# Optimization experiments

Measured on AMD Instinct MI355X. Metric: run time of the kernel, lower is better.

## Reference

```python
import jax, jax.numpy as jnp
import numpy as np

B, M, IN_DIM, D, H, NL = 4, 2048, 512, 1024, 4, 2
HD = D // H           # head_dim = 256
HD2 = HD // 2
ROPE_BASE = 10000.0
LN_EPS = 1e-5


def setup_inputs() -> dict:
    key = jax.random.key(0)
    ks = jax.random.split(key, 9)
    s = 0.02
    return {
        "x": jax.random.normal(ks[0], (B, M, IN_DIM), jnp.float32),
        "positions": jnp.sort(jax.random.randint(ks[1], (B, M), 0, 8192), axis=-1).astype(jnp.int32),
        "mask": jnp.ones((B, M), jnp.float32),
        "in_w": jax.random.normal(ks[2], (IN_DIM, D), jnp.float32) * s,
        "in_b": jnp.zeros((D,), jnp.float32),
        "qkv_w": jax.random.normal(ks[3], (NL, D, 3 * D), jnp.float32) * s,
        "o_w": jax.random.normal(ks[4], (NL, D, D), jnp.float32) * s,
        "ln1_g": jnp.ones((NL, D), jnp.float32),
        "ln1_b": jnp.zeros((NL, D), jnp.float32),
        "ffn_w1": jax.random.normal(ks[5], (NL, D, 4 * D), jnp.float32) * s,
        "ffn_b1": jnp.zeros((NL, 4 * D), jnp.float32),
        "ffn_w2": jax.random.normal(ks[6], (NL, 4 * D, D), jnp.float32) * s,
        "ffn_b2": jnp.zeros((NL, D), jnp.float32),
        "ln2_g": jnp.ones((NL, D), jnp.float32),
        "ln2_b": jnp.zeros((NL, D), jnp.float32),
        "start_state": jax.random.normal(ks[7], (D,), jnp.float32) * 0.02,
    }


def _layernorm(x, g, b):
    mu = jnp.mean(x, axis=-1, keepdims=True)
    var = jnp.mean((x - mu) ** 2, axis=-1, keepdims=True)
    return (x - mu) * jax.lax.rsqrt(var + LN_EPS) * g + b


def _rope_cos_sin(positions):
    # rope_module(pos): angles over head_dim//2 freqs, shared across heads
    inv_freq = 1.0 / (ROPE_BASE ** (jnp.arange(HD2, dtype=jnp.float32) * 2.0 / HD))
    ang = positions.astype(jnp.float32)[:, :, None] * inv_freq  # (B, L, HD2)
    return jnp.cos(ang), jnp.sin(ang)


def _apply_rotary(x, cos, sin):
    # x: (B, H, L, HD); cos/sin: (B, 1, L, HD2) broadcast over heads
    x1, x2 = x[..., :HD2], x[..., HD2:]
    return jnp.concatenate([x1 * cos - x2 * sin, x1 * sin + x2 * cos], axis=-1)


def _self_attention(x, cos, sin, mask, qkv_w, o_w):
    Bx, L, Dx = x.shape
    qkv = (x @ qkv_w).reshape(Bx, L, 3, H, HD)
    q = jnp.transpose(qkv[:, :, 0], (0, 2, 1, 3))  # (B, H, L, HD)
    k = jnp.transpose(qkv[:, :, 1], (0, 2, 1, 3))
    v = jnp.transpose(qkv[:, :, 2], (0, 2, 1, 3))
    q = _apply_rotary(q, cos, sin)
    k = _apply_rotary(k, cos, sin)
    scores = jnp.einsum("bhqd,bhkd->bhqk", q, k) * (1.0 / np.sqrt(HD))
    scores = jnp.where(mask[:, None, None, :] == 0, -jnp.inf, scores)
    attn = jax.nn.softmax(scores, axis=-1)
    out = jnp.einsum("bhqk,bhkd->bhqd", attn, v)
    out = jnp.transpose(out, (0, 2, 1, 3)).reshape(Bx, L, Dx)
    return out @ o_w


def reference(x, positions, mask, in_w, in_b, qkv_w, o_w, ln1_g, ln1_b,
              ffn_w1, ffn_b1, ffn_w2, ffn_b2, ln2_g, ln2_b, start_state):
    h = x @ in_w + in_b  # (B, M, D)
    cos, sin = _rope_cos_sin(positions)
    cos, sin = cos[:, None], sin[:, None]  # (B, 1, M, HD2)
    for l in range(NL):
        h = h + _self_attention(_layernorm(h, ln1_g[l], ln1_b[l]), cos, sin, mask,
                                qkv_w[l], o_w[l])
        y = _layernorm(h, ln2_g[l], ln2_b[l])
        y = jax.nn.gelu(y @ ffn_w1[l] + ffn_b1[l], approximate=False) @ ffn_w2[l] + ffn_b2[l]
        h = h + y
    lengths = jnp.sum(mask, axis=1)
    last_idx = jnp.clip(lengths.astype(jnp.int32) - 1, 0, None)
    gathered = h[jnp.arange(h.shape[0]), last_idx]  # (B, D)
    has_hist = lengths > 0
    return jnp.where(has_hist[:, None], gathered, start_state[None, :])
```

## Files before the change

### kernel.cpp

```cpp
#include <hip/hip_runtime.h>
#include <math.h>

typedef __attribute__((ext_vector_type(8))) short bf16x8;
typedef __attribute__((ext_vector_type(4))) float floatx4;
typedef __attribute__((ext_vector_type(4))) unsigned short ushort4v;

typedef __attribute__((address_space(1))) void as1_void;
typedef __attribute__((address_space(3))) void as3_void;

static __device__ __forceinline__ unsigned short f2b(float f) {
    union { float f; unsigned u; } v; v.f = f;
    unsigned r = v.u + 0x7fffu + ((v.u >> 16) & 1u);
    return (unsigned short)(r >> 16);
}
static __device__ __forceinline__ float b2f(unsigned short h) {
    union { unsigned u; float f; } v; v.u = ((unsigned)h) << 16;
    return v.f;
}

template<int TM, int TN>
__global__ __launch_bounds__(256) void gemm_bf16(
    const unsigned short* __restrict__ A,
    const unsigned short* __restrict__ Bt,
    float* __restrict__ Cf, unsigned short* __restrict__ Cb,
    const float* __restrict__ bias,
    int K, int lda, int ldb, int ldc,
    int zdiv, long a_s1, long a_s2, long b_s1, long b_s2, long c_s1, long c_s2,
    int mode)
{
    constexpr int FM  = TM / 32;
    constexpr int FN  = TN / 32;
    constexpr int NRA = TM / 64;
    constexpr int NRB = TN / 64;
    constexpr int NSTG = NRA + NRB;

    __shared__ unsigned short As[2][4 * TM * 8];
    __shared__ unsigned short Bs[2][4 * TN * 8];

    const int tid  = threadIdx.x;
    const int wid  = tid >> 6;
    const int lane = tid & 63;
    const int q    = lane >> 4;
    const int r    = lane & 15;

    const int z  = blockIdx.z;
    const int zq = z / zdiv, zr = z % zdiv;
    const long offC = (long)zq * c_s1 + (long)zr * c_s2;

    const int m0 = blockIdx.y * TM;
    const int n0 = blockIdx.x * TN;

    const unsigned short* Ab = A  + (long)zq * a_s1 + (long)zr * a_s2 + (long)m0 * lda;
    const unsigned short* Bb = Bt + (long)zq * b_s1 + (long)zr * b_s2 + (long)n0 * ldb;

    const int wr = (wid >> 1) * (TM / 2);
    const int wc = (wid & 1)  * (TN / 2);

    floatx4 acc[FM][FN];
    #pragma unroll
    for (int i = 0; i < FM; ++i)
        #pragma unroll
        for (int j = 0; j < FN; ++j)
            acc[i][j] = (floatx4){0.f, 0.f, 0.f, 0.f};

    const int qc = wid;
    const int nk = K >> 5;

    auto stage = [&](int kt, int buf) {
        const int kofs = (kt << 5) + (qc << 3);
        #pragma unroll
        for (int rb = 0; rb < NRA; ++rb)
            __builtin_amdgcn_global_load_lds(
                (as1_void*)(void*)(Ab + (long)(lane + rb * 64) * lda + kofs),
                (as3_void*)&As[buf][(qc * TM + rb * 64) * 8], 16, 0, 0);
        #pragma unroll
        for (int rb = 0; rb < NRB; ++rb)
            __builtin_amdgcn_global_load_lds(
                (as1_void*)(void*)(Bb + (long)(lane + rb * 64) * ldb + kofs),
                (as3_void*)&Bs[buf][(qc * TN + rb * 64) * 8], 16, 0, 0);
    };

    stage(0, 0);
    for (int kt = 0; kt < nk; ++kt) {
        const int cur = kt & 1;
        if (kt + 1 < nk) {
            stage(kt + 1, cur ^ 1);
            if constexpr (NSTG == 2)      asm volatile("s_waitcnt vmcnt(2)" ::: "memory");
            else if constexpr (NSTG == 4) asm volatile("s_waitcnt vmcnt(4)" ::: "memory");
            else if constexpr (NSTG == 6) asm volatile("s_waitcnt vmcnt(6)" ::: "memory");
            else                          asm volatile("s_waitcnt vmcnt(0)" ::: "memory");
        } else {
            asm volatile("s_waitcnt vmcnt(0)" ::: "memory");
        }
        asm volatile("s_barrier" ::: "memory");

        bf16x8 av[FM], bv[FN];
        #pragma unroll
        for (int i = 0; i < FM; ++i)
            av[i] = *(const bf16x8*)&As[cur][(q * TM + wr + i * 16 + r) * 8];
        #pragma unroll
        for (int j = 0; j < FN; ++j)
            bv[j] = *(const bf16x8*)&Bs[cur][(q * TN + wc + j * 16 + r) * 8];
        #pragma unroll
        for (int i = 0; i < FM; ++i)
            #pragma unroll
            for (int j = 0; j < FN; ++j)
                acc[i][j] = __builtin_amdgcn_mfma_f32_16x16x32_bf16(av[i], bv[j], acc[i][j], 0, 0, 0);

        asm volatile("s_waitcnt lgkmcnt(0)" ::: "memory");
        asm volatile("s_barrier" ::: "memory");
    }

    #pragma unroll
    for (int i = 0; i < FM; ++i) {
        const int gr0 = m0 + wr + i * 16 + q * 4;
        #pragma unroll
        for (int j = 0; j < FN; ++j) {
            const int gc = n0 + wc + j * 16 + r;
            const float bvl = bias ? bias[gc] : 0.0f;
            #pragma unroll
            for (int rr = 0; rr < 4; ++rr) {
                const long cidx = offC + (long)(gr0 + rr) * ldc + gc;
                float v = acc[i][j][rr] + bvl;
                if (mode == 0) {
                    Cf[cidx] = v;
                } else if (mode == 1) {
                    Cf[cidx] += v;
                } else if (mode == 2) {
                    Cb[cidx] = f2b(v);
                } else {
                    Cb[cidx] = f2b(0.5f * v * (1.0f + erff(v * 0.70710678118654752f)));
                }
            }
        }
    }
}

__global__ void transpose_cast_f32(const float* __restrict__ in, unsigned short* __restrict__ out,
                                   int R, int C)
{
    __shared__ float t[32][33];
    const int c0 = blockIdx.x * 32, r0 = blockIdx.y * 32;
    const int tx = threadIdx.x, ty = threadIdx.y;
    #pragma unroll
    for (int i = 0; i < 4; ++i)
        t[ty + i * 8][tx] = in[(long)(r0 + ty + i * 8) * C + c0 + tx];
    __syncthreads();
    #pragma unroll
    for (int i = 0; i < 4; ++i)
        out[(long)(c0 + ty + i * 8) * R + r0 + tx] = f2b(t[tx][ty + i * 8]);
}

__global__ void transpose_v(const unsigned short* __restrict__ qkv, unsigned short* __restrict__ vT)
{
    __shared__ unsigned short t[32][33];
    const int hh = blockIdx.z;
    const int d0 = blockIdx.x * 32, m0 = blockIdx.y * 32;
    const int tx = threadIdx.x, ty = threadIdx.y;
    const unsigned short* ip = qkv + 2048 + hh * 256;
    unsigned short* op = vT + (long)hh * 524288;
    #pragma unroll
    for (int i = 0; i < 4; ++i)
        t[ty + i * 8][tx] = ip[(long)(m0 + ty + i * 8) * 3072 + d0 + tx];
    __syncthreads();
    #pragma unroll
    for (int i = 0; i < 4; ++i)
        op[(long)(d0 + ty + i * 8) * 2048 + m0 + tx] = t[tx][ty + i * 8];
}

__global__ void cast_f32_bf16(const float* __restrict__ in, unsigned short* __restrict__ out)
{
    const long i = (long)blockIdx.x * 256 + threadIdx.x;
    const float4 v = ((const float4*)in)[i];
    ushort4v o;
    o[0] = f2b(v.x); o[1] = f2b(v.y); o[2] = f2b(v.z); o[3] = f2b(v.w);
    ((ushort4v*)out)[i] = o;
}

__global__ void zero_f32(float* __restrict__ p)
{
    p[blockIdx.x * 256 + threadIdx.x] = 0.0f;
}

__global__ __launch_bounds__(256) void ln_kernel(const float* __restrict__ h,
    const float* __restrict__ g, const float* __restrict__ bta,
    unsigned short* __restrict__ out)
{
    const int tok = blockIdx.x;
    const float4 v = ((const float4*)(h + (long)tok * 1024))[threadIdx.x];
    float s  = v.x + v.y + v.z + v.w;
    float s2 = v.x * v.x + v.y * v.y + v.z * v.z + v.w * v.w;
    #pragma unroll
    for (int off = 32; off > 0; off >>= 1) {
        s  += __shfl_xor(s, off);
        s2 += __shfl_xor(s2, off);
    }
    __shared__ float rs[4], rs2[4];
    const int wid = threadIdx.x >> 6, lane = threadIdx.x & 63;
    if (lane == 0) { rs[wid] = s; rs2[wid] = s2; }
    __syncthreads();
    s  = rs[0] + rs[1] + rs[2] + rs[3];
    s2 = rs2[0] + rs2[1] + rs2[2] + rs2[3];
    const float mu = s * (1.0f / 1024.0f);
    float var = s2 * (1.0f / 1024.0f) - mu * mu;
    var = fmaxf(var, 0.0f);
    const float rsg = 1.0f / sqrtf(var + 1e-5f);
    const float4 gv = ((const float4*)g)[threadIdx.x];
    const float4 bv = ((const float4*)bta)[threadIdx.x];
    ushort4v o;
    o[0] = f2b((v.x - mu) * rsg * gv.x + bv.x);
    o[1] = f2b((v.y - mu) * rsg * gv.y + bv.y);
    o[2] = f2b((v.z - mu) * rsg * gv.z + bv.z);
    o[3] = f2b((v.w - mu) * rsg * gv.w + bv.w);
    *(ushort4v*)&out[(long)tok * 1024 + threadIdx.x * 4] = o;
}

__global__ __launch_bounds__(256) void rope_kernel(unsigned short* __restrict__ qkv,
                                                   const int* __restrict__ pos)
{
    const int tok = blockIdx.x;
    const float p = (float)pos[tok];
    unsigned short* base = qkv + (long)tok * 3072;
    const float kC = -13.287712379549449f / 128.0f;
    #pragma unroll
    for (int it = 0; it < 2; ++it) {
        const int idx = threadIdx.x + it * 256;
        const int hh = idx >> 7, d = idx & 127;
        const float inv = exp2f((float)d * kC);
        const float ang = p * inv;
        const float c = cosf(ang), s = sinf(ang);
        unsigned short* qp = base + hh * 256 + d;
        {
            const float x1 = b2f(qp[0]), x2 = b2f(qp[128]);
            qp[0]   = f2b(x1 * c - x2 * s);
            qp[128] = f2b(x1 * s + x2 * c);
        }
        unsigned short* kp = qp + 1024;
        {
            const float x1 = b2f(kp[0]), x2 = b2f(kp[128]);
            kp[0]   = f2b(x1 * c - x2 * s);
            kp[128] = f2b(x1 * s + x2 * c);
        }
    }
}

__global__ __launch_bounds__(256) void softmax_kernel(unsigned short* __restrict__ sc,
                                                      const float* __restrict__ mrow)
{
    unsigned short* row = sc + (long)blockIdx.x * 2048;
    const int t = threadIdx.x;

    float v[8];
    const ushort4v u0 = *(const ushort4v*)&row[t * 8];
    const ushort4v u1 = *(const ushort4v*)&row[t * 8 + 4];
    #pragma unroll
    for (int i = 0; i < 4; ++i) { v[i] = b2f(u0[i]); v[4 + i] = b2f(u1[i]); }

    const float4 m0 = ((const float4*)mrow)[t * 2];
    const float4 m1 = ((const float4*)mrow)[t * 2 + 1];
    float mk[8] = {m0.x, m0.y, m0.z, m0.w, m1.x, m1.y, m1.z, m1.w};

    float mx = -3.0e38f;
    #pragma unroll
    for (int i = 0; i < 8; ++i) {
        v[i] = (mk[i] == 0.0f) ? -3.0e38f : v[i] * 0.0625f;
        mx = fmaxf(mx, v[i]);
    }
    #pragma unroll
    for (int off = 32; off > 0; off >>= 1) mx = fmaxf(mx, __shfl_xor(mx, off));
    __shared__ float rmx[4], rsm[4];
    const int wid = t >> 6, lane = t & 63;
    if (lane == 0) rmx[wid] = mx;
    __syncthreads();
    mx = fmaxf(fmaxf(rmx[0], rmx[1]), fmaxf(rmx[2], rmx[3]));

    float s = 0.0f;
    #pragma unroll
    for (int i = 0; i < 8; ++i) { v[i] = expf(v[i] - mx); s += v[i]; }
    #pragma unroll
    for (int off = 32; off > 0; off >>= 1) s += __shfl_xor(s, off);
    if (lane == 0) rsm[wid] = s;
    __syncthreads();
    s = rsm[0] + rsm[1] + rsm[2] + rsm[3];
    const float invs = (s > 0.0f) ? 1.0f / s : 0.0f;

    ushort4v o0, o1;
    #pragma unroll
    for (int i = 0; i < 4; ++i) { o0[i] = f2b(v[i] * invs); o1[i] = f2b(v[4 + i] * invs); }
    *(ushort4v*)&row[t * 8]     = o0;
    *(ushort4v*)&row[t * 8 + 4] = o1;
}

__global__ __launch_bounds__(256) void gather_kernel(const float* __restrict__ h,
    const float* __restrict__ mask, const float* __restrict__ ss, float* __restrict__ out)
{
    const int b = blockIdx.x;
    const float* mrow = mask + b * 2048;
    const int t = threadIdx.x;
    float s = 0.0f;
    #pragma unroll
    for (int i = 0; i < 8; ++i) s += mrow[t * 8 + i];
    #pragma unroll
    for (int off = 32; off > 0; off >>= 1) s += __shfl_xor(s, off);
    __shared__ float red[4];
    if ((t & 63) == 0) red[t >> 6] = s;
    __syncthreads();
    const float len = red[0] + red[1] + red[2] + red[3];
    const int L = (int)len;
    const int last = (L > 0) ? (L - 1) : 0;
    const bool has = len > 0.0f;
    const float* src = has ? (h + ((long)b * 2048 + last) * 1024) : ss;
    #pragma unroll
    for (int i = 0; i < 4; ++i) {
        const int d = t + i * 256;
        out[b * 1024 + d] = src[d];
    }
}

extern "C" void kernel_launch(void* const* d_in, const int* in_sizes, int n_in,
                              void* d_out, int out_size, void* d_ws, size_t ws_size,
                              hipStream_t stream)
{
    (void)in_sizes; (void)n_in; (void)out_size;
    const float* x      = (const float*)d_in[0];
    const int*   pos    = (const int*)d_in[1];
    const float* mask   = (const float*)d_in[2];
    const float* in_w   = (const float*)d_in[3];
    const float* in_b   = (const float*)d_in[4];
    const float* qkv_w  = (const float*)d_in[5];
    const float* o_w    = (const float*)d_in[6];
    const float* ln1_g  = (const float*)d_in[7];
    const float* ln1_b  = (const float*)d_in[8];
    const float* ffn_w1 = (const float*)d_in[9];
    const float* ffn_b1 = (const float*)d_in[10];
    const float* ffn_w2 = (const float*)d_in[11];
    const float* ffn_b2 = (const float*)d_in[12];
    const float* ln2_g  = (const float*)d_in[13];
    const float* ln2_b  = (const float*)d_in[14];
    const float* sstate = (const float*)d_in[15];
    float* out = (float*)d_out;

    const size_t NEED = 143654912ull;
    if (ws_size < NEED) {
        zero_f32<<<16, 256, 0, stream>>>(out);
        return;
    }
    char* w = (char*)d_ws;
    unsigned short* wt_in  = (unsigned short*)(w);
    unsigned short* wt_qkv = (unsigned short*)(w + 1048576);
    unsigned short* wt_o   = (unsigned short*)(w + 7340032);
    unsigned short* wt_f1  = (unsigned short*)(w + 9437184);
    unsigned short* wt_f2  = (unsigned short*)(w + 17825792);
    float*          hbuf   = (float*)(w + 26214400);
    unsigned short* xn_bf  = (unsigned short*)(w + 59768832);
    unsigned short* ao_bf  = (unsigned short*)(w + 76546048);
    unsigned short* qkv_b  = (unsigned short*)(w + 93323264);
    unsigned short* vT_b   = (unsigned short*)(w + 105906176);
    unsigned short* scmid  = (unsigned short*)(w + 110100480);
    unsigned short* x_bf   = ao_bf;
    unsigned short* mid_bf = (unsigned short*)(w + 76546048);

    const dim3 tb(32, 8);

    transpose_cast_f32<<<dim3(32, 16), tb, 0, stream>>>(in_w, wt_in, 512, 1024);
    cast_f32_bf16<<<4096, 256, 0, stream>>>(x, x_bf);

    gemm_bf16<128,128><<<dim3(8, 64, 1), 256, 0, stream>>>(x_bf, wt_in, hbuf, nullptr, in_b,
        512, 512, 512, 1024, 1, 0, 0, 0, 0, 0, 0, 0);

    for (int l = 0; l < 2; ++l) {
        transpose_cast_f32<<<dim3(96, 32),  tb, 0, stream>>>(qkv_w  + (long)l * 3145728, wt_qkv, 1024, 3072);
        transpose_cast_f32<<<dim3(32, 32),  tb, 0, stream>>>(o_w    + (long)l * 1048576, wt_o,   1024, 1024);
        transpose_cast_f32<<<dim3(128, 32), tb, 0, stream>>>(ffn_w1 + (long)l * 4194304, wt_f1,  1024, 4096);
        transpose_cast_f32<<<dim3(32, 128), tb, 0, stream>>>(ffn_w2 + (long)l * 4194304, wt_f2,  4096, 1024);

        ln_kernel<<<8192, 256, 0, stream>>>(hbuf, ln1_g + l * 1024, ln1_b + l * 1024, xn_bf);

        for (int b = 0; b < 4; ++b) {
            gemm_bf16<64,64><<<dim3(48, 32, 1), 256, 0, stream>>>(xn_bf + (long)b * 2097152, wt_qkv,
                nullptr, qkv_b, nullptr, 1024, 1024, 1024, 3072, 1, 0, 0, 0, 0, 0, 0, 2);
            rope_kernel<<<2048, 256, 0, stream>>>(qkv_b, pos + b * 2048);
            transpose_v<<<dim3(8, 64, 4), tb, 0, stream>>>(qkv_b, vT_b);
            gemm_bf16<128,128><<<dim3(16, 16, 4), 256, 0, stream>>>(qkv_b, qkv_b + 1024,
                nullptr, scmid, nullptr, 256, 3072, 3072, 2048,
                1, 256l, 0, 256l, 0, 4194304l, 0, 2);
            softmax_kernel<<<8192, 256, 0, stream>>>(scmid, mask + b * 2048);
            gemm_bf16<64,64><<<dim3(4, 32, 4), 256, 0, stream>>>(scmid, vT_b,
                nullptr, ao_bf + (long)b * 2097152, nullptr, 2048, 2048, 2048, 1024,
                1, 4194304l, 0, 524288l, 0, 256l, 0, 2);
        }
        gemm_bf16<128,128><<<dim3(8, 64, 1), 256, 0, stream>>>(ao_bf, wt_o,
            hbuf, nullptr, nullptr, 1024, 1024, 1024, 1024, 1, 0, 0, 0, 0, 0, 0, 1);

        ln_kernel<<<8192, 256, 0, stream>>>(hbuf, ln2_g + l * 1024, ln2_b + l * 1024, xn_bf);

        gemm_bf16<256,128><<<dim3(32, 32, 1), 256, 0, stream>>>(xn_bf, wt_f1,
            nullptr, mid_bf, ffn_b1 + l * 4096, 1024, 1024, 1024, 4096, 1, 0, 0, 0, 0, 0, 0, 3);
        gemm_bf16<128,128><<<dim3(8, 64, 1), 256, 0, stream>>>(mid_bf, wt_f2,
            hbuf, nullptr, ffn_b2 + l * 1024, 4096, 4096, 4096, 1024, 1, 0, 0, 0, 0, 0, 0, 1);
    }

    gather_kernel<<<4, 256, 0, stream>>>(hbuf, mask, sstate, out);
}
```

Before: 2.516 ms.

## Retune GEMM tile shapes and make layernorm one token per wavefront

Several GEMM launches switch to different tile shapes: in-proj, o-proj and FFN2 go to 128x64, QKV goes to 64x128, and FFN1 goes to 128x128. The main intent is more workgroups per launch and better CU occupancy. The layernorm kernel now handles one token per 64-lane wavefront with four tokens per block, which removes the LDS reduction and __syncthreads. The vmcnt wait table gains an NSTG==3 case (needed for the new tile combos) and drops NSTG==6. Smaller tiles trade load balance for less data reuse per tile.

```diff
diff --git a/kernel.cpp b/kernel.cpp
--- a/kernel.cpp
+++ b/kernel.cpp
@@ -86,8 +86,8 @@
         if (kt + 1 < nk) {
             stage(kt + 1, cur ^ 1);
             if constexpr (NSTG == 2)      asm volatile("s_waitcnt vmcnt(2)" ::: "memory");
+            else if constexpr (NSTG == 3) asm volatile("s_waitcnt vmcnt(3)" ::: "memory");
             else if constexpr (NSTG == 4) asm volatile("s_waitcnt vmcnt(4)" ::: "memory");
-            else if constexpr (NSTG == 6) asm volatile("s_waitcnt vmcnt(6)" ::: "memory");
             else                          asm volatile("s_waitcnt vmcnt(0)" ::: "memory");
         } else {
             asm volatile("s_waitcnt vmcnt(0)" ::: "memory");
@@ -186,33 +186,40 @@
     const float* __restrict__ g, const float* __restrict__ bta,
     unsigned short* __restrict__ out)
 {
-    const int tok = blockIdx.x;
-    const float4 v = ((const float4*)(h + (long)tok * 1024))[threadIdx.x];
-    float s  = v.x + v.y + v.z + v.w;
-    float s2 = v.x * v.x + v.y * v.y + v.z * v.z + v.w * v.w;
+    const int wid  = threadIdx.x >> 6;
+    const int lane = threadIdx.x & 63;
+    const long tok = (long)blockIdx.x * 4 + wid;
+    const float4* h4 = (const float4*)(h + tok * 1024);
+
+    float4 v[4];
+    float s = 0.f, s2 = 0.f;
+    #pragma unroll
+    for (int i = 0; i < 4; ++i) {
+        v[i] = h4[lane + i * 64];
+        s  += v[i].x + v[i].y + v[i].z + v[i].w;
+        s2 += v[i].x * v[i].x + v[i].y * v[i].y + v[i].z * v[i].z + v[i].w * v[i].w;
+    }
     #pragma unroll
     for (int off = 32; off > 0; off >>= 1) {
         s  += __shfl_xor(s, off);
         s2 += __shfl_xor(s2, off);
     }
-    __shared__ float rs[4], rs2[4];
-    const int wid = threadIdx.x >> 6, lane = threadIdx.x & 63;
-    if (lane == 0) { rs[wid] = s; rs2[wid] = s2; }
-    __syncthreads();
-    s  = rs[0] + rs[1] + rs[2] + rs[3];
-    s2 = rs2[0] + rs2[1] + rs2[2] + rs2[3];
     const float mu = s * (1.0f / 1024.0f);
     float var = s2 * (1.0f / 1024.0f) - mu * mu;
     var = fmaxf(var, 0.0f);
     const float rsg = 1.0f / sqrtf(var + 1e-5f);
-    const float4 gv = ((const float4*)g)[threadIdx.x];
-    const float4 bv = ((const float4*)bta)[threadIdx.x];
-    ushort4v o;
-    o[0] = f2b((v.x - mu) * rsg * gv.x + bv.x);
-    o[1] = f2b((v.y - mu) * rsg * gv.y + bv.y);
-    o[2] = f2b((v.z - mu) * rsg * gv.z + bv.z);
-    o[3] = f2b((v.w - mu) * rsg * gv.w + bv.w);
-    *(ushort4v*)&out[(long)tok * 1024 + threadIdx.x * 4] = o;
+
+    #pragma unroll
+    for (int i = 0; i < 4; ++i) {
+        const float4 gv = ((const float4*)g)[lane + i * 64];
+        const float4 bv = ((const float4*)bta)[lane + i * 64];
+        ushort4v o;
+        o[0] = f2b((v[i].x - mu) * rsg * gv.x + bv.x);
+        o[1] = f2b((v[i].y - mu) * rsg * gv.y + bv.y);
+        o[2] = f2b((v[i].z - mu) * rsg * gv.z + bv.z);
+        o[3] = f2b((v[i].w - mu) * rsg * gv.w + bv.w);
+        *(ushort4v*)&out[tok * 1024 + (lane + i * 64) * 4] = o;
+    }
 }
 
 __global__ __launch_bounds__(256) void rope_kernel(unsigned short* __restrict__ qkv,
@@ -365,7 +372,7 @@
     transpose_cast_f32<<<dim3(32, 16), tb, 0, stream>>>(in_w, wt_in, 512, 1024);
     cast_f32_bf16<<<4096, 256, 0, stream>>>(x, x_bf);
 
-    gemm_bf16<128,128><<<dim3(8, 64, 1), 256, 0, stream>>>(x_bf, wt_in, hbuf, nullptr, in_b,
+    gemm_bf16<128,64><<<dim3(16, 64, 1), 256, 0, stream>>>(x_bf, wt_in, hbuf, nullptr, in_b,
         512, 512, 512, 1024, 1, 0, 0, 0, 0, 0, 0, 0);
 
     for (int l = 0; l < 2; ++l) {
@@ -374,10 +381,10 @@
         transpose_cast_f32<<<dim3(128, 32), tb, 0, stream>>>(ffn_w1 + (long)l * 4194304, wt_f1,  1024, 4096);
         transpose_cast_f32<<<dim3(32, 128), tb, 0, stream>>>(ffn_w2 + (long)l * 4194304, wt_f2,  4096, 1024);
 
-        ln_kernel<<<8192, 256, 0, stream>>>(hbuf, ln1_g + l * 1024, ln1_b + l * 1024, xn_bf);
+        ln_kernel<<<2048, 256, 0, stream>>>(hbuf, ln1_g + l * 1024, ln1_b + l * 1024, xn_bf);
 
         for (int b = 0; b < 4; ++b) {
-            gemm_bf16<64,64><<<dim3(48, 32, 1), 256, 0, stream>>>(xn_bf + (long)b * 2097152, wt_qkv,
+            gemm_bf16<64,128><<<dim3(24, 32, 1), 256, 0, stream>>>(xn_bf + (long)b * 2097152, wt_qkv,
                 nullptr, qkv_b, nullptr, 1024, 1024, 1024, 3072, 1, 0, 0, 0, 0, 0, 0, 2);
             rope_kernel<<<2048, 256, 0, stream>>>(qkv_b, pos + b * 2048);
             transpose_v<<<dim3(8, 64, 4), tb, 0, stream>>>(qkv_b, vT_b);
@@ -389,14 +396,14 @@
                 nullptr, ao_bf + (long)b * 2097152, nullptr, 2048, 2048, 2048, 1024,
                 1, 4194304l, 0, 524288l, 0, 256l, 0, 2);
         }
-        gemm_bf16<128,128><<<dim3(8, 64, 1), 256, 0, stream>>>(ao_bf, wt_o,
+        gemm_bf16<128,64><<<dim3(16, 64, 1), 256, 0, stream>>>(ao_bf, wt_o,
             hbuf, nullptr, nullptr, 1024, 1024, 1024, 1024, 1, 0, 0, 0, 0, 0, 0, 1);
 
-        ln_kernel<<<8192, 256, 0, stream>>>(hbuf, ln2_g + l * 1024, ln2_b + l * 1024, xn_bf);
-
-        gemm_bf16<256,128><<<dim3(32, 32, 1), 256, 0, stream>>>(xn_bf, wt_f1,
+        ln_kernel<<<2048, 256, 0, stream>>>(hbuf, ln2_g + l * 1024, ln2_b + l * 1024, xn_bf);
+
+        gemm_bf16<128,128><<<dim3(32, 64, 1), 256, 0, stream>>>(xn_bf, wt_f1,
             nullptr, mid_bf, ffn_b1 + l * 4096, 1024, 1024, 1024, 4096, 1, 0, 0, 0, 0, 0, 0, 3);
-        gemm_bf16<128,128><<<dim3(8, 64, 1), 256, 0, stream>>>(mid_bf, wt_f2,
+        gemm_bf16<128,64><<<dim3(16, 64, 1), 256, 0, stream>>>(mid_bf, wt_f2,
             hbuf, nullptr, ffn_b2 + l * 1024, 4096, 4096, 4096, 1024, 1, 0, 0, 0, 0, 0, 0, 1);
     }
 
```

After: 2.318 ms. 1.09x faster.
